# Performance work log

Measured on AMD Instinct MI355X. Metric: run time of the kernel, lower is better.

The kernel has to match this reference:

```python
import jax, jax.numpy as jnp
import numpy as np

B, T, C = 2, 4096, 768
H = 12
D = C // H  # head_dim = 64


def setup_inputs() -> dict:
    key = jax.random.key(0)
    kx, kq, kk, kv, ko = jax.random.split(key, 5)
    s = 1.0 / np.sqrt(C)  # keep activations well-scaled
    return {
        "x": jax.random.normal(kx, (B, T, C), dtype=jnp.float32),
        "wq": jax.random.normal(kq, (C, C), dtype=jnp.float32) * s,
        "wk": jax.random.normal(kk, (C, C), dtype=jnp.float32) * s,
        "wv": jax.random.normal(kv, (C, C), dtype=jnp.float32) * s,
        "wo": jax.random.normal(ko, (C, C), dtype=jnp.float32) * s,
    }


def reference(x, wq, wk, wv, wo):
    b, t, c = x.shape
    # projections (torch Linear: y = x @ W.T); split heads -> (B,H,T,D)
    q = (x @ wq.T).reshape(b, t, H, D).transpose(0, 2, 1, 3)
    k = (x @ wk.T).reshape(b, t, H, D).transpose(0, 2, 1, 3)
    v = (x @ wv.T).reshape(b, t, H, D).transpose(0, 2, 1, 3)
    scale = 1.0 / jnp.sqrt(jnp.asarray(D, dtype=x.dtype))
    scores = jnp.einsum("bhqd,bhkd->bhqk", q, k) * scale  # (B,H,T,T)
    causal = jnp.tril(jnp.ones((t, t), dtype=bool))
    scores = jnp.where(causal, scores, jnp.asarray(-jnp.inf, dtype=scores.dtype))
    attn = jax.nn.softmax(scores, axis=-1)
    ctx = jnp.einsum("bhqk,bhkd->bhqd", attn, v)  # (B,H,T,D)
    ctx = ctx.transpose(0, 2, 1, 3).reshape(b, t, c)
    return ctx @ wo.T
```

## Files before the change

### kernel.cpp

```cpp
#include <hip/hip_runtime.h>
#include <hip/hip_bf16.h>

#define B_  2
#define T_  4096
#define C_  768
#define H_  12
#define D_  64
#define MTOT (B_*T_)

typedef __bf16 bf16;
typedef __bf16 bf16x8 __attribute__((ext_vector_type(8)));
typedef __bf16 bf16x4 __attribute__((ext_vector_type(4)));
typedef float  f32x4  __attribute__((ext_vector_type(4)));
typedef unsigned int u32x4 __attribute__((ext_vector_type(4)));

__device__ __forceinline__ void gl_lds16(const bf16* g, bf16* l) {
    __builtin_amdgcn_global_load_lds(
        (const __attribute__((address_space(1))) void*)g,
        (__attribute__((address_space(3))) void*)l, 16, 0, 0);
}

__device__ __forceinline__ void pswap32_16(unsigned int& x, unsigned int& y) {
    auto r1 = __builtin_amdgcn_permlane32_swap(x, y, false, false);
    auto r2 = __builtin_amdgcn_permlane16_swap(r1[0], r1[1], false, false);
    x = r2[0]; y = r2[1];
}
__device__ __forceinline__ unsigned int cvtpk(float lo, float hi) {
    unsigned int r;
    asm("v_cvt_pk_bf16_f32 %0, %1, %2" : "=v"(r) : "v"(lo), "v"(hi));
    return r;
}

__global__ __launch_bounds__(256) void cvt_bf16(const float* __restrict__ src,
                                                bf16* __restrict__ dst, int n8) {
    int i = blockIdx.x * 256 + threadIdx.x;
    if (i >= n8) return;
    const float4* s4 = (const float4*)src;
    float4 a = s4[2*(size_t)i], b = s4[2*(size_t)i+1];
    bf16x8 o;
    o[0]=(bf16)a.x; o[1]=(bf16)a.y; o[2]=(bf16)a.z; o[3]=(bf16)a.w;
    o[4]=(bf16)b.x; o[5]=(bf16)b.y; o[6]=(bf16)b.z; o[7]=(bf16)b.w;
    *(bf16x8*)(dst + 8*(size_t)i) = o;
}

__global__ __launch_bounds__(256) void cvt_bf16_w4(const float* __restrict__ w0,
                                                   const float* __restrict__ w1,
                                                   const float* __restrict__ w2,
                                                   const float* __restrict__ w3,
                                                   bf16* __restrict__ d0,
                                                   bf16* __restrict__ d1,
                                                   bf16* __restrict__ d2,
                                                   bf16* __restrict__ d3) {
    int z = blockIdx.y;
    const float* src = (z==0)?w0:(z==1)?w1:(z==2)?w2:w3;
    bf16* dst = (z==0)?d0:(z==1)?d1:(z==2)?d2:d3;
    int i = blockIdx.x * 256 + threadIdx.x;
    const float4* s4 = (const float4*)src;
    float4 a = s4[2*(size_t)i], b = s4[2*(size_t)i+1];
    bf16x8 o;
    o[0]=(bf16)a.x; o[1]=(bf16)a.y; o[2]=(bf16)a.z; o[3]=(bf16)a.w;
    o[4]=(bf16)b.x; o[5]=(bf16)b.y; o[6]=(bf16)b.z; o[7]=(bf16)b.w;
    *(bf16x8*)(dst + 8*(size_t)i) = o;
}

__global__ __launch_bounds__(256) void gemm_qkv(const bf16* __restrict__ xb,
                                                const bf16* __restrict__ wqb,
                                                const bf16* __restrict__ wkb,
                                                const bf16* __restrict__ wvb,
                                                bf16* __restrict__ qo,
                                                bf16* __restrict__ ko,
                                                bf16* __restrict__ vto) {
    int z = blockIdx.z;
    const bf16* w = (z == 0) ? wqb : (z == 1) ? wkb : wvb;
    bf16* dst = (z == 0) ? qo : (z == 1) ? ko : vto;
    int mbase = blockIdx.x * 128;
    int nbase = blockIdx.y * 128;
    __shared__ bf16 As[2][128][32];
    __shared__ bf16 Bs[2][128][32];
    int tid  = threadIdx.x;
    int wave = tid >> 6, lane = tid & 63;
    int wm = (wave >> 1) * 64, wn = (wave & 1) * 64;
    int lr = lane & 15, lg = lane >> 4;
    int srow0 = tid >> 2, scol0 = tid & 3;
    int srow1 = (tid + 256) >> 2, scol1 = (tid + 256) & 3;
    const bf16* xa0 = xb + (size_t)(mbase + srow0) * C_ + scol0 * 8;
    const bf16* xa1 = xb + (size_t)(mbase + srow1) * C_ + scol1 * 8;
    const bf16* wa0 = w  + (size_t)(nbase + srow0) * C_ + scol0 * 8;
    const bf16* wa1 = w  + (size_t)(nbase + srow1) * C_ + scol1 * 8;
#define GSTAGE(kb_, cb_) do { \
        gl_lds16(xa0 + (kb_), &As[cb_][srow0][scol0 * 8]); \
        gl_lds16(xa1 + (kb_), &As[cb_][srow1][scol1 * 8]); \
        gl_lds16(wa0 + (kb_), &Bs[cb_][srow0][scol0 * 8]); \
        gl_lds16(wa1 + (kb_), &Bs[cb_][srow1][scol1 * 8]); \
    } while (0)
    f32x4 acc[4][4] = {};
    GSTAGE(0, 0);
    __syncthreads();
    int cur = 0;
    for (int kb = 0; kb < C_; kb += 32) {
        if (kb + 32 < C_) GSTAGE(kb + 32, cur ^ 1);
        bf16x8 af[4], bfr[4];
        #pragma unroll
        for (int mt = 0; mt < 4; ++mt) af[mt]  = *(const bf16x8*)(&As[cur][wm + mt*16 + lr][lg*8]);
        #pragma unroll
        for (int nt = 0; nt < 4; ++nt) bfr[nt] = *(const bf16x8*)(&Bs[cur][wn + nt*16 + lr][lg*8]);
        #pragma unroll
        for (int mt = 0; mt < 4; ++mt)
            #pragma unroll
            for (int nt = 0; nt < 4; ++nt)
                acc[mt][nt] = __builtin_amdgcn_mfma_f32_16x16x32_bf16(af[mt], bfr[nt], acc[mt][nt], 0, 0, 0);
        __syncthreads();
        cur ^= 1;
    }
#undef GSTAGE
    float sc = (z == 0) ? 0.18033688011112042f : 1.0f;
    int m0 = mbase + wm + (lg << 2);
    int n0 = nbase + wn + lr;
    if (z < 2) {
        #pragma unroll
        for (int mt = 0; mt < 4; ++mt) {
            #pragma unroll
            for (int nt = 0; nt < 4; ++nt) {
                int n = n0 + nt * 16;
                int h = n >> 6, d = n & 63;
                #pragma unroll
                for (int r = 0; r < 4; ++r) {
                    int m = m0 + mt * 16 + r;
                    int b = m >> 12, t = m & 4095;
                    dst[(((size_t)b * H_ + h) * T_ + t) * 64 + d] = (bf16)(acc[mt][nt][r] * sc);
                }
            }
        }
    } else {
        #pragma unroll
        for (int mt = 0; mt < 4; ++mt) {
            int m = m0 + mt * 16;
            int b = m >> 12, t = m & 4095;
            #pragma unroll
            for (int nt = 0; nt < 4; ++nt) {
                int n = n0 + nt * 16;
                int h = n >> 6, d = n & 63;
                bf16x4 pk;
                #pragma unroll
                for (int r = 0; r < 4; ++r) pk[r] = (bf16)acc[mt][nt][r];
                *(bf16x4*)(dst + (((size_t)b * H_ + h) * 64 + d) * T_ + t) = pk;
            }
        }
    }
}

__global__ __launch_bounds__(256) void gemm_out(const bf16* __restrict__ ctx,
                                                const bf16* __restrict__ wob,
                                                float* __restrict__ out) {
    int mbase = blockIdx.x * 128;
    int nbase = blockIdx.y * 128;
    __shared__ bf16 As[2][128][32];
    __shared__ bf16 Bs[2][128][32];
    int tid  = threadIdx.x;
    int wave = tid >> 6, lane = tid & 63;
    int wm = (wave >> 1) * 64, wn = (wave & 1) * 64;
    int lr = lane & 15, lg = lane >> 4;
    int srow0 = tid >> 2, scol0 = tid & 3;
    int srow1 = (tid + 256) >> 2, scol1 = (tid + 256) & 3;
    const bf16* xa0 = ctx + (size_t)(mbase + srow0) * C_ + scol0 * 8;
    const bf16* xa1 = ctx + (size_t)(mbase + srow1) * C_ + scol1 * 8;
    const bf16* wa0 = wob + (size_t)(nbase + srow0) * C_ + scol0 * 8;
    const bf16* wa1 = wob + (size_t)(nbase + srow1) * C_ + scol1 * 8;
#define GSTAGE(kb_, cb_) do { \
        gl_lds16(xa0 + (kb_), &As[cb_][srow0][scol0 * 8]); \
        gl_lds16(xa1 + (kb_), &As[cb_][srow1][scol1 * 8]); \
        gl_lds16(wa0 + (kb_), &Bs[cb_][srow0][scol0 * 8]); \
        gl_lds16(wa1 + (kb_), &Bs[cb_][srow1][scol1 * 8]); \
    } while (0)
    f32x4 acc[4][4] = {};
    GSTAGE(0, 0);
    __syncthreads();
    int cur = 0;
    for (int kb = 0; kb < C_; kb += 32) {
        if (kb + 32 < C_) GSTAGE(kb + 32, cur ^ 1);
        bf16x8 af[4], bfr[4];
        #pragma unroll
        for (int mt = 0; mt < 4; ++mt) af[mt]  = *(const bf16x8*)(&As[cur][wm + mt*16 + lr][lg*8]);
        #pragma unroll
        for (int nt = 0; nt < 4; ++nt) bfr[nt] = *(const bf16x8*)(&Bs[cur][wn + nt*16 + lr][lg*8]);
        #pragma unroll
        for (int mt = 0; mt < 4; ++mt)
            #pragma unroll
            for (int nt = 0; nt < 4; ++nt)
                acc[mt][nt] = __builtin_amdgcn_mfma_f32_16x16x32_bf16(af[mt], bfr[nt], acc[mt][nt], 0, 0, 0);
        __syncthreads();
        cur ^= 1;
    }
#undef GSTAGE
    int m0 = mbase + wm + (lg << 2);
    int n0 = nbase + wn + lr;
    #pragma unroll
    for (int mt = 0; mt < 4; ++mt)
        #pragma unroll
        for (int nt = 0; nt < 4; ++nt)
            #pragma unroll
            for (int r = 0; r < 4; ++r)
                out[(size_t)(m0 + mt * 16 + r) * C_ + n0 + nt * 16] = acc[mt][nt][r];
}

__device__ __forceinline__ void attn_store(const f32x4 (&o)[4], float l, bf16* __restrict__ ctx,
                                           int b, int qrow, int h, int lg) {
    float inv = 1.0f / l;
    #pragma unroll
    for (int dt = 0; dt < 4; ++dt) {
        bf16x4 pk;
        #pragma unroll
        for (int r = 0; r < 4; ++r) pk[r] = (bf16)(o[dt][r] * inv);
        *(bf16x4*)(ctx + ((size_t)b * T_ + qrow) * C_ + h * 64 + dt * 16 + lg * 4) = pk;
    }
}

__global__ __launch_bounds__(256) void attn(const bf16* __restrict__ q,
                                            const bf16* __restrict__ k,
                                            const bf16* __restrict__ vt,
                                            bf16* __restrict__ ctx) {
    int idx = blockIdx.x;
    int qt = 63 - idx / 24;
    int bh = idx % 24;
    int b = bh / H_, h = bh % H_;
    int tid = threadIdx.x;
    int wave = tid >> 6, lane = tid & 63;
    int lr = lane & 15, lg = lane >> 4;

    __shared__ bf16 Ks[2][64][64];
    __shared__ bf16 Vs[2][64][64];

    const bf16* qp = q  + (size_t)bh * T_ * 64;
    const bf16* kp = k  + (size_t)bh * T_ * 64;
    const bf16* vp = vt + (size_t)bh * 64 * (size_t)T_;

    int r0 = tid >> 3, c0 = tid & 7;
    int cs = (c0 ^ (r0 & 7)) * 8;
    const bf16* kstg = kp + (size_t)r0 * 64 + cs;
    const bf16* vstg = vp + (size_t)r0 * T_ + cs;

#define STAGE(kb_, cb_) do { \
        const bf16* ks_ = kstg + (size_t)(kb_) * 64 * 64; \
        const bf16* vs_ = vstg + (size_t)(kb_) * 64; \
        gl_lds16(ks_,                   &Ks[cb_][r0][c0 * 8]); \
        gl_lds16(ks_ + 32 * 64,         &Ks[cb_][32 + r0][c0 * 8]); \
        gl_lds16(vs_,                   &Vs[cb_][r0][c0 * 8]); \
        gl_lds16(vs_ + (size_t)32 * T_, &Vs[cb_][32 + r0][c0 * 8]); \
    } while (0)

    const float NEGINF = -__builtin_inff();

    int qb = qt * 64 + wave * 16;
    int n  = qt + 1;
    int qrow = qb + lr;

    int sw = lr & 7;
    int col0 = (lg ^ sw) * 8;
    int col1 = ((4 | lg) ^ sw) * 8;

    bf16x8 qf[2];
    #pragma unroll
    for (int c = 0; c < 2; ++c)
        qf[c] = *(const bf16x8*)(qp + (size_t)(qb + lr) * 64 + c * 32 + lg * 8);

    u32x4 onep;
    onep[0] = 0x3F803F80u; onep[1] = 0x3F803F80u; onep[2] = 0x3F803F80u; onep[3] = 0x3F803F80u;
    bf16x8 ones = __builtin_bit_cast(bf16x8, onep);

    f32x4 o[4] = {};
    f32x4 lacc = {};
    const f32x4 fz = {};

    STAGE(0, 0);
    __syncthreads();
    int cur = 0;

    for (int kb = 0; kb < n; ++kb) {
        int kv = kb * 64;
        if (kb + 1 < n) STAGE(kb + 1, cur ^ 1);

        f32x4 s[4];
        __builtin_amdgcn_s_setprio(1);
        #pragma unroll
        for (int nt = 0; nt < 4; ++nt) {
            bf16x8 kf0 = *(const bf16x8*)(&Ks[cur][nt * 16 + lr][col0]);
            s[nt] = __builtin_amdgcn_mfma_f32_16x16x32_bf16(kf0, qf[0], fz, 0, 0, 0);
        }
        #pragma unroll
        for (int nt = 0; nt < 4; ++nt) {
            bf16x8 kf1 = *(const bf16x8*)(&Ks[cur][nt * 16 + lr][col1]);
            s[nt] = __builtin_amdgcn_mfma_f32_16x16x32_bf16(kf1, qf[1], s[nt], 0, 0, 0);
        }
        __builtin_amdgcn_s_setprio(0);
        if (kb == qt) {
            #pragma unroll
            for (int nt = 0; nt < 4; ++nt)
                #pragma unroll
                for (int r = 0; r < 4; ++r) {
                    int key = kv + nt * 16 + lg * 4 + r;
                    s[nt][r] = (key > qrow) ? NEGINF : s[nt][r];
                }
        }
        #pragma unroll
        for (int nt = 0; nt < 4; ++nt)
            #pragma unroll
            for (int r = 0; r < 4; ++r)
                s[nt][r] = __builtin_amdgcn_exp2f(s[nt][r]);
        unsigned int dpk[8];
        #pragma unroll
        for (int nt = 0; nt < 4; ++nt) {
            dpk[2*nt]   = cvtpk(s[nt][0], s[nt][1]);
            dpk[2*nt+1] = cvtpk(s[nt][2], s[nt][3]);
        }
        unsigned int pw[2][4];
        #pragma unroll
        for (int c2 = 0; c2 < 2; ++c2)
            #pragma unroll
            for (int pr = 0; pr < 2; ++pr) {
                unsigned int x = dpk[4*c2 + pr], y = dpk[4*c2 + 2 + pr];
                pswap32_16(x, y);
                pw[c2][pr] = x;
                pw[c2][2+pr] = y;
            }
        __builtin_amdgcn_s_setprio(1);
        #pragma unroll
        for (int c2 = 0; c2 < 2; ++c2) {
            u32x4 pt;
            pt[0] = pw[c2][0]; pt[1] = pw[c2][1]; pt[2] = pw[c2][2]; pt[3] = pw[c2][3];
            bf16x8 pf = __builtin_bit_cast(bf16x8, pt);
            int vcol = c2 ? col1 : col0;
            #pragma unroll
            for (int dt = 0; dt < 4; ++dt) {
                bf16x8 vfr = *(const bf16x8*)(&Vs[cur][dt * 16 + lr][vcol]);
                o[dt] = __builtin_amdgcn_mfma_f32_16x16x32_bf16(vfr, pf, o[dt], 0, 0, 0);
            }
            lacc = __builtin_amdgcn_mfma_f32_16x16x32_bf16(ones, pf, lacc, 0, 0, 0);
        }
        __builtin_amdgcn_s_setprio(0);

        __syncthreads();
        cur ^= 1;
    }
#undef STAGE

    attn_store(o, lacc[0], ctx, b, qrow, h, lg);
}

extern "C" void kernel_launch(void* const* d_in, const int* in_sizes, int n_in,
                              void* d_out, int out_size, void* d_ws, size_t ws_size,
                              hipStream_t stream) {
    const float* x  = (const float*)d_in[0];
    const float* wq = (const float*)d_in[1];
    const float* wk = (const float*)d_in[2];
    const float* wv = (const float*)d_in[3];
    const float* wo = (const float*)d_in[4];
    float* out = (float*)d_out;

    char* ws = (char*)d_ws;
    const size_t SZ_XB = (size_t)MTOT * C_ * sizeof(bf16);
    const size_t SZ_W  = (size_t)C_ * C_ * sizeof(bf16);
    bf16* xb  = (bf16*)(ws);
    bf16* wqb = (bf16*)(ws + SZ_XB);
    bf16* wkb = (bf16*)(ws + SZ_XB + SZ_W);
    bf16* wvb = (bf16*)(ws + SZ_XB + 2 * SZ_W);
    bf16* wob = (bf16*)(ws + SZ_XB + 3 * SZ_W);
    bf16* qb  = (bf16*)(ws + SZ_XB + 4 * SZ_W);
    bf16* kb  = (bf16*)(ws + 2 * SZ_XB + 4 * SZ_W);
    bf16* vtb = (bf16*)(ws + 3 * SZ_XB + 4 * SZ_W);
    bf16* ctb = (bf16*)(ws + 4 * SZ_XB + 4 * SZ_W);

    cvt_bf16<<<3072, 256, 0, stream>>>(x, xb, MTOT * C_ / 8);
    cvt_bf16_w4<<<dim3(288, 4), 256, 0, stream>>>(wq, wk, wv, wo, wqb, wkb, wvb, wob);

    gemm_qkv<<<dim3(MTOT / 128, C_ / 128, 3), 256, 0, stream>>>(xb, wqb, wkb, wvb, qb, kb, vtb);
    attn<<<1536, 256, 0, stream>>>(qb, kb, vtb, ctb);
    gemm_out<<<dim3(MTOT / 128, C_ / 128), 256, 0, stream>>>(ctb, wob, out);
}
```

Measured before the change: 227.6 us.

## Pair low and high causal query tiles per block to balance work and share KV

Each attention block now handles two query tiles, qlo and 63-qlo, so every block does the same total causal work, and the grid is halved to 768 blocks. For key blocks up to qlo, the staged K/V tiles in LDS are reused by both query tiles, with interleaved MFMAs. The remaining key blocks serve only the high tile. This removes tail imbalance and redundant K/V loads, at the cost of more registers and fewer blocks in flight.

```diff
diff --git a/kernel.cpp b/kernel.cpp
--- a/kernel.cpp
+++ b/kernel.cpp
@@ -220,8 +220,9 @@
                                             const bf16* __restrict__ vt,
                                             bf16* __restrict__ ctx) {
     int idx = blockIdx.x;
-    int qt = 63 - idx / 24;
-    int bh = idx % 24;
+    int qlo = idx / 24;
+    int qhi = 63 - qlo;
+    int bh  = idx % 24;
     int b = bh / H_, h = bh % H_;
     int tid = threadIdx.x;
     int wave = tid >> 6, lane = tid & 63;
@@ -250,33 +251,124 @@
 
     const float NEGINF = -__builtin_inff();
 
-    int qb = qt * 64 + wave * 16;
-    int n  = qt + 1;
-    int qrow = qb + lr;
+    int qbA = qlo * 64 + wave * 16;
+    int qbB = qhi * 64 + wave * 16;
+    int qrowA = qbA + lr, qrowB = qbB + lr;
+    int n = qhi + 1;
 
     int sw = lr & 7;
     int col0 = (lg ^ sw) * 8;
     int col1 = ((4 | lg) ^ sw) * 8;
 
-    bf16x8 qf[2];
+    bf16x8 qfA[2], qfB[2];
     #pragma unroll
-    for (int c = 0; c < 2; ++c)
-        qf[c] = *(const bf16x8*)(qp + (size_t)(qb + lr) * 64 + c * 32 + lg * 8);
+    for (int c = 0; c < 2; ++c) {
+        qfA[c] = *(const bf16x8*)(qp + (size_t)(qbA + lr) * 64 + c * 32 + lg * 8);
+        qfB[c] = *(const bf16x8*)(qp + (size_t)(qbB + lr) * 64 + c * 32 + lg * 8);
+    }
 
     u32x4 onep;
     onep[0] = 0x3F803F80u; onep[1] = 0x3F803F80u; onep[2] = 0x3F803F80u; onep[3] = 0x3F803F80u;
     bf16x8 ones = __builtin_bit_cast(bf16x8, onep);
 
-    f32x4 o[4] = {};
-    f32x4 lacc = {};
+    f32x4 oA[4] = {}, oB[4] = {};
+    f32x4 laccA = {}, laccB = {};
     const f32x4 fz = {};
 
     STAGE(0, 0);
     __syncthreads();
     int cur = 0;
 
-    for (int kb = 0; kb < n; ++kb) {
-        int kv = kb * 64;
+    for (int kb = 0; kb <= qlo; ++kb) {
+        if (kb + 1 < n) STAGE(kb + 1, cur ^ 1);
+
+        f32x4 sA[4], sB[4];
+        __builtin_amdgcn_s_setprio(1);
+        #pragma unroll
+        for (int nt = 0; nt < 4; ++nt) {
+            bf16x8 kf0 = *(const bf16x8*)(&Ks[cur][nt * 16 + lr][col0]);
+            sB[nt] = __builtin_amdgcn_mfma_f32_16x16x32_bf16(kf0, qfB[0], fz, 0, 0, 0);
+            sA[nt] = __builtin_amdgcn_mfma_f32_16x16x32_bf16(kf0, qfA[0], fz, 0, 0, 0);
+        }
+        #pragma unroll
+        for (int nt = 0; nt < 4; ++nt) {
+            bf16x8 kf1 = *(const bf16x8*)(&Ks[cur][nt * 16 + lr][col1]);
+            sB[nt] = __builtin_amdgcn_mfma_f32_16x16x32_bf16(kf1, qfB[1], sB[nt], 0, 0, 0);
+            sA[nt] = __builtin_amdgcn_mfma_f32_16x16x32_bf16(kf1, qfA[1], sA[nt], 0, 0, 0);
+        }
+        __builtin_amdgcn_s_setprio(0);
+        if (kb == qlo) {
+            int kv = kb * 64;
+            #pragma unroll
+            for (int nt = 0; nt < 4; ++nt)
+                #pragma unroll
+                for (int r = 0; r < 4; ++r) {
+                    int key = kv + nt * 16 + lg * 4 + r;
+                    sA[nt][r] = (key > qrowA) ? NEGINF : sA[nt][r];
+                }
+        }
+        #pragma unroll
+        for (int nt = 0; nt < 4; ++nt)
+            #pragma unroll
+            for (int r = 0; r < 4; ++r) {
+                sB[nt][r] = __builtin_amdgcn_exp2f(sB[nt][r]);
+                sA[nt][r] = __builtin_amdgcn_exp2f(sA[nt][r]);
+            }
+        unsigned int pwA[2][4], pwB[2][4];
+        {
+            unsigned int dpk[8];
+            #pragma unroll
+            for (int nt = 0; nt < 4; ++nt) {
+                dpk[2*nt]   = cvtpk(sB[nt][0], sB[nt][1]);
+                dpk[2*nt+1] = cvtpk(sB[nt][2], sB[nt][3]);
+            }
+            #pragma unroll
+            for (int c2 = 0; c2 < 2; ++c2)
+                #pragma unroll
+                for (int pr = 0; pr < 2; ++pr) {
+                    unsigned int x = dpk[4*c2 + pr], y = dpk[4*c2 + 2 + pr];
+                    pswap32_16(x, y);
+                    pwB[c2][pr] = x; pwB[c2][2+pr] = y;
+                }
+            #pragma unroll
+            for (int nt = 0; nt < 4; ++nt) {
+                dpk[2*nt]   = cvtpk(sA[nt][0], sA[nt][1]);
+                dpk[2*nt+1] = cvtpk(sA[nt][2], sA[nt][3]);
+            }
+            #pragma unroll
+            for (int c2 = 0; c2 < 2; ++c2)
+                #pragma unroll
+                for (int pr = 0; pr < 2; ++pr) {
+                    unsigned int x = dpk[4*c2 + pr], y = dpk[4*c2 + 2 + pr];
+                    pswap32_16(x, y);
+                    pwA[c2][pr] = x; pwA[c2][2+pr] = y;
+                }
+        }
+        __builtin_amdgcn_s_setprio(1);
+        #pragma unroll
+        for (int c2 = 0; c2 < 2; ++c2) {
+            u32x4 ptB, ptA;
+            ptB[0]=pwB[c2][0]; ptB[1]=pwB[c2][1]; ptB[2]=pwB[c2][2]; ptB[3]=pwB[c2][3];
+            ptA[0]=pwA[c2][0]; ptA[1]=pwA[c2][1]; ptA[2]=pwA[c2][2]; ptA[3]=pwA[c2][3];
+            bf16x8 pfB = __builtin_bit_cast(bf16x8, ptB);
+            bf16x8 pfA = __builtin_bit_cast(bf16x8, ptA);
+            int vcol = c2 ? col1 : col0;
+            #pragma unroll
+            for (int dt = 0; dt < 4; ++dt) {
+                bf16x8 vfr = *(const bf16x8*)(&Vs[cur][dt * 16 + lr][vcol]);
+                oB[dt] = __builtin_amdgcn_mfma_f32_16x16x32_bf16(vfr, pfB, oB[dt], 0, 0, 0);
+                oA[dt] = __builtin_amdgcn_mfma_f32_16x16x32_bf16(vfr, pfA, oA[dt], 0, 0, 0);
+            }
+            laccB = __builtin_amdgcn_mfma_f32_16x16x32_bf16(ones, pfB, laccB, 0, 0, 0);
+            laccA = __builtin_amdgcn_mfma_f32_16x16x32_bf16(ones, pfA, laccA, 0, 0, 0);
+        }
+        __builtin_amdgcn_s_setprio(0);
+
+        __syncthreads();
+        cur ^= 1;
+    }
+
+    for (int kb = qlo + 1; kb < n; ++kb) {
         if (kb + 1 < n) STAGE(kb + 1, cur ^ 1);
 
         f32x4 s[4];
@@ -284,21 +376,22 @@
         #pragma unroll
         for (int nt = 0; nt < 4; ++nt) {
             bf16x8 kf0 = *(const bf16x8*)(&Ks[cur][nt * 16 + lr][col0]);
-            s[nt] = __builtin_amdgcn_mfma_f32_16x16x32_bf16(kf0, qf[0], fz, 0, 0, 0);
+            s[nt] = __builtin_amdgcn_mfma_f32_16x16x32_bf16(kf0, qfB[0], fz, 0, 0, 0);
         }
         #pragma unroll
         for (int nt = 0; nt < 4; ++nt) {
             bf16x8 kf1 = *(const bf16x8*)(&Ks[cur][nt * 16 + lr][col1]);
-            s[nt] = __builtin_amdgcn_mfma_f32_16x16x32_bf16(kf1, qf[1], s[nt], 0, 0, 0);
+            s[nt] = __builtin_amdgcn_mfma_f32_16x16x32_bf16(kf1, qfB[1], s[nt], 0, 0, 0);
         }
         __builtin_amdgcn_s_setprio(0);
-        if (kb == qt) {
+        if (kb == qhi) {
+            int kv = kb * 64;
             #pragma unroll
             for (int nt = 0; nt < 4; ++nt)
                 #pragma unroll
                 for (int r = 0; r < 4; ++r) {
                     int key = kv + nt * 16 + lg * 4 + r;
-                    s[nt][r] = (key > qrow) ? NEGINF : s[nt][r];
+                    s[nt][r] = (key > qrowB) ? NEGINF : s[nt][r];
                 }
         }
         #pragma unroll
@@ -319,8 +412,7 @@
             for (int pr = 0; pr < 2; ++pr) {
                 unsigned int x = dpk[4*c2 + pr], y = dpk[4*c2 + 2 + pr];
                 pswap32_16(x, y);
-                pw[c2][pr] = x;
-                pw[c2][2+pr] = y;
+                pw[c2][pr] = x; pw[c2][2+pr] = y;
             }
         __builtin_amdgcn_s_setprio(1);
         #pragma unroll
@@ -332,9 +424,9 @@
             #pragma unroll
             for (int dt = 0; dt < 4; ++dt) {
                 bf16x8 vfr = *(const bf16x8*)(&Vs[cur][dt * 16 + lr][vcol]);
-                o[dt] = __builtin_amdgcn_mfma_f32_16x16x32_bf16(vfr, pf, o[dt], 0, 0, 0);
-            }
-            lacc = __builtin_amdgcn_mfma_f32_16x16x32_bf16(ones, pf, lacc, 0, 0, 0);
+                oB[dt] = __builtin_amdgcn_mfma_f32_16x16x32_bf16(vfr, pf, oB[dt], 0, 0, 0);
+            }
+            laccB = __builtin_amdgcn_mfma_f32_16x16x32_bf16(ones, pf, laccB, 0, 0, 0);
         }
         __builtin_amdgcn_s_setprio(0);
 
@@ -343,7 +435,8 @@
     }
 #undef STAGE
 
-    attn_store(o, lacc[0], ctx, b, qrow, h, lg);
+    attn_store(oA, laccA[0], ctx, b, qrowA, h, lg);
+    attn_store(oB, laccB[0], ctx, b, qrowB, h, lg);
 }
 
 extern "C" void kernel_launch(void* const* d_in, const int* in_sizes, int n_in,
@@ -373,6 +466,6 @@
     cvt_bf16_w4<<<dim3(288, 4), 256, 0, stream>>>(wq, wk, wv, wo, wqb, wkb, wvb, wob);
 
     gemm_qkv<<<dim3(MTOT / 128, C_ / 128, 3), 256, 0, stream>>>(xb, wqb, wkb, wvb, qb, kb, vtb);
-    attn<<<1536, 256, 0, stream>>>(qb, kb, vtb, ctb);
+    attn<<<768, 256, 0, stream>>>(qb, kb, vtb, ctb);
     gemm_out<<<dim3(MTOT / 128, C_ / 128), 256, 0, stream>>>(ctb, wob, out);
 }
```

Result: faster. 219.4 us (-3.6%).
